# Kernel tuning notes

Hardware: AMD Instinct MI355X
Metric: run time of the kernel (lower is better)

## Reference

```python
import jax, jax.numpy as jnp
import numpy as np

N_NODES = 10000
N_EDGES = 320000
D = 128  # feature dim for edges, nodes, globals


def setup_inputs() -> dict:
    key = jax.random.key(0)
    ks = jax.random.split(key, 8)
    edges = jax.random.normal(ks[0], (N_EDGES, D), dtype=jnp.float32)
    nodes = jax.random.normal(ks[1], (N_NODES, D), dtype=jnp.float32)
    globals_ = jax.random.normal(ks[2], (D,), dtype=jnp.float32)
    receivers = jax.random.randint(ks[3], (N_EDGES,), 0, N_NODES, dtype=jnp.int32).astype(jnp.int64)
    senders = jax.random.randint(ks[4], (N_EDGES,), 0, N_NODES, dtype=jnp.int32).astype(jnp.int64)
    W1 = jax.random.normal(ks[5], (4 * D, 256), dtype=jnp.float32) * (1.0 / np.sqrt(4 * D))
    b1 = jnp.zeros((256,), dtype=jnp.float32)
    W2 = jax.random.normal(ks[6], (256, D), dtype=jnp.float32) * (1.0 / np.sqrt(256))
    b2 = jnp.zeros((D,), dtype=jnp.float32)
    return {"edges": edges, "nodes": nodes, "globals_": globals_,
            "receivers": receivers, "senders": senders,
            "W1": W1, "b1": b1, "W2": W2, "b2": b2}


def reference(edges, nodes, globals_, receivers, senders, W1, b1, W2, b2):
    # Gather adjacent node features to edges, broadcast globals, concat.
    recv_feats = nodes[receivers]                 # [E, D]
    send_feats = nodes[senders]                   # [E, D]
    glob_feats = jnp.broadcast_to(globals_, (edges.shape[0], globals_.shape[0]))  # [E, D]
    x = jnp.concatenate([edges, recv_feats, send_feats, glob_feats], axis=-1)     # [E, 4D]
    # Edge-update MLP: 4D -> 256 -> D with relu.
    h = jax.nn.relu(x @ W1 + b1)
    new_edges = h @ W2 + b2                       # [E, D]
    return new_edges
```

## Files before the change

### kernel.cpp

```cpp
#include <hip/hip_runtime.h>
#include <hip/hip_bf16.h>

#define D 128
#define NH 256
#define BM 64
#define E_TOTAL 320000
#define NNODES 10000

typedef __attribute__((ext_vector_type(8))) short bf16x8;
typedef __attribute__((ext_vector_type(4))) float f32x4;

__device__ __forceinline__ unsigned short f2b(float f) {
  unsigned int u = __builtin_bit_cast(unsigned int, f);
  u += 0x7fffu + ((u >> 16) & 1u);
  return (unsigned short)(u >> 16);
}
__device__ __forceinline__ unsigned pk2(float a, float b) {
  return (unsigned)f2b(a) | ((unsigned)f2b(b) << 16);
}
__device__ __forceinline__ uint4 pack8(float4 a, float4 b) {
  uint4 r;
  r.x = pk2(a.x, a.y); r.y = pk2(a.z, a.w);
  r.z = pk2(b.x, b.y); r.w = pk2(b.z, b.w);
  return r;
}
__device__ __forceinline__ float lo2f(unsigned u) {
  return __builtin_bit_cast(float, u << 16);
}
__device__ __forceinline__ float hi2f(unsigned u) {
  return __builtin_bit_cast(float, u & 0xffff0000u);
}
__device__ __forceinline__ void gload16(const void* g, void* l) {
  __builtin_amdgcn_global_load_lds(
      (const __attribute__((address_space(1))) void*)g,
      (__attribute__((address_space(3))) void*)l, 16, 0, 0);
}

__global__ void prep_kernel(const float* __restrict__ W1,
                            const float* __restrict__ W2,
                            const float* __restrict__ b1,
                            const float* __restrict__ g,
                            ushort* __restrict__ W1pk,
                            ushort* __restrict__ W2p,
                            float* __restrict__ cvec) {
  const int b = blockIdx.x;
  const int tid = threadIdx.x;
  if (b < 48) {
    int c = b * 256 + tid;
    int s = c >> 12;
    int rem = c & 4095;
    int nt = rem >> 8;
    int rem2 = rem & 255;
    int ks = rem2 >> 6;
    int l = rem2 & 63;
    int col = nt * 16 + (l & 15);
    int k0 = s * 128 + ks * 32 + (l >> 4) * 8;
    ushort* dst = W1pk + (size_t)c * 8;
    #pragma unroll
    for (int j = 0; j < 8; ++j)
      dst[j] = f2b(W1[(size_t)(k0 + j) * NH + col]);
  } else if (b < 64) {
    int c = (b - 48) * 256 + tid;
    int nt2 = c / (8 * 64);
    int rem = c % (8 * 64);
    int ks = rem >> 6;
    int l = rem & 63;
    int col = nt2 * 16 + (l & 15);
    int k0 = ks * 32 + (l >> 4) * 8;
    ushort* dst = W2p + (size_t)c * 8;
    #pragma unroll
    for (int j = 0; j < 8; ++j)
      dst[j] = f2b(W2[(size_t)(k0 + j) * D + col]);
  } else {
    int n = tid;
    float acc = b1[n];
    for (int k = 0; k < D; ++k)
      acc += g[k] * W1[(size_t)(384 + k) * NH + n];
    cvec[n] = acc;
  }
}

__global__ __launch_bounds__(512, 4) void nodeh_kernel(
    const float* __restrict__ nodes,
    const ushort* __restrict__ W1pk,
    const float* __restrict__ cvec,
    ushort* __restrict__ tblR,
    ushort* __restrict__ tblS) {
  __shared__ char Xn[BM * 256];
  const int role = blockIdx.y;
  ushort* __restrict__ tbl = role ? tblS : tblR;
  const int nb = blockIdx.x * BM;
  const int tid = threadIdx.x;

  {
    int row = tid >> 4;
    int cc = (tid & 15) * 16;
    #pragma unroll
    for (int q = 0; q < 2; ++q) {
      int r = row + q * 32;
      int rg = nb + r; if (rg >= NNODES) rg = NNODES - 1;
      const float* np = nodes + (size_t)rg * D + (tid & 15) * 8;
      float4 u0 = *(const float4*)np;
      float4 u1 = *(const float4*)(np + 4);
      *(uint4*)(Xn + r * 256 + (cc ^ ((r & 7) << 4))) = pack8(u0, u1);
    }
  }
  __syncthreads();

  const int lane = tid & 63;
  const int wave = tid >> 6;
  const int lr = lane & 15;
  const int kg = lane >> 4;

  const ushort* wb = W1pk + (size_t)(1 + role) * 32768
                   + (size_t)(wave * 2) * 2048 + lane * 8;
  f32x4 acc[2][4] = {};
  bf16x8 aw[2][2];
  #pragma unroll
  for (int ht = 0; ht < 2; ++ht)
    aw[0][ht] = *(const bf16x8*)(wb + ht * 2048);

  #pragma unroll
  for (int ks = 0; ks < 4; ++ks) {
    const int cur = ks & 1, nxt = cur ^ 1;
    if (ks < 3) {
      #pragma unroll
      for (int ht = 0; ht < 2; ++ht)
        aw[nxt][ht] = *(const bf16x8*)(wb + ht * 2048 + (ks + 1) * 512);
    }
    const int k0 = ks * 32 + kg * 8;
    bf16x8 xb[4];
    #pragma unroll
    for (int et = 0; et < 4; ++et) {
      int row = et * 16 + lr;
      xb[et] = *(const bf16x8*)(Xn + row * 256 + ((k0 * 2) ^ ((row & 7) << 4)));
    }
    #pragma unroll
    for (int ht = 0; ht < 2; ++ht)
      #pragma unroll
      for (int et = 0; et < 4; ++et)
        acc[ht][et] = __builtin_amdgcn_mfma_f32_16x16x32_bf16(aw[cur][ht], xb[et], acc[ht][et], 0, 0, 0);
  }

  #pragma unroll
  for (int ht = 0; ht < 2; ++ht) {
    int h0 = wave * 32 + ht * 16 + kg * 4;
    float4 cvq = {0.f, 0.f, 0.f, 0.f};
    if (role == 0) cvq = *(const float4*)(cvec + h0);
    #pragma unroll
    for (int et = 0; et < 4; ++et) {
      int n = nb + et * 16 + lr;
      if (n < NNODES) {
        uint2 pk;
        pk.x = pk2(acc[ht][et][0] + cvq.x, acc[ht][et][1] + cvq.y);
        pk.y = pk2(acc[ht][et][2] + cvq.z, acc[ht][et][3] + cvq.w);
        *(uint2*)(tbl + (size_t)n * NH + h0) = pk;
      }
    }
  }
}

__global__ __launch_bounds__(512, 4) void fused_kernel(
    const float* __restrict__ edges,
    const int* __restrict__ receivers,
    const int* __restrict__ senders,
    const ushort* __restrict__ W1pk,
    const ushort* __restrict__ tblR,
    const ushort* __restrict__ tblS,
    const ushort* __restrict__ W2p,
    const float* __restrict__ b2,
    float* __restrict__ out) {
  __shared__ char Xs[BM * 256];
  __shared__ char Hr[BM * 512];
  __shared__ char Hsb[BM * 512];

  const int ebase = blockIdx.x * BM;
  const int tid = threadIdx.x;
  const int lane = tid & 63;
  const int wave = tid >> 6;

  {
    const int wslice = wave & 3;
    const int isS = wave >> 2;
    const int* __restrict__ myarr = isS ? senders : receivers;
    const char* mytbl = (const char*)(isS ? tblS : tblR);
    char* myLds = isS ? Hsb : Hr;
    const int half = lane >> 5;
    const int ch16 = (lane & 31) * 16;
    #pragma unroll
    for (int j = 0; j < 8; ++j) {
      int r = wslice * 16 + 2 * j + half;
      int idx = myarr[ebase + r];
      gload16(mytbl + (size_t)idx * 512 + (ch16 ^ ((r & 7) << 4)),
              myLds + (wslice * 16 + 2 * j) * 512);
    }
  }

  const int erow = tid >> 4;
  const int ecc = (tid & 15) * 16;
  {
    const float* ep0 = edges + (size_t)(ebase + erow) * D + (tid & 15) * 8;
    float4 e0 = *(const float4*)ep0;
    float4 e1 = *(const float4*)(ep0 + 4);
    const float* ep1 = edges + (size_t)(ebase + erow + 32) * D + (tid & 15) * 8;
    float4 e2 = *(const float4*)ep1;
    float4 e3 = *(const float4*)(ep1 + 4);
    *(uint4*)(Xs + erow * 256 + (ecc ^ ((erow & 7) << 4))) = pack8(e0, e1);
    int r2 = erow + 32;
    *(uint4*)(Xs + r2 * 256 + (ecc ^ ((r2 & 7) << 4))) = pack8(e2, e3);
  }
  __syncthreads();

  const int lr = lane & 15;
  const int kg = lane >> 4;

  const ushort* w1base = W1pk + (size_t)(wave * 2) * 2048 + lane * 8;
  f32x4 acc[2][4] = {};
  bf16x8 aw[2][2];
  #pragma unroll
  for (int ht = 0; ht < 2; ++ht)
    aw[0][ht] = *(const bf16x8*)(w1base + ht * 2048);

  #pragma unroll
  for (int ks = 0; ks < 4; ++ks) {
    const int cur = ks & 1, nxt = cur ^ 1;
    if (ks < 3) {
      #pragma unroll
      for (int ht = 0; ht < 2; ++ht)
        aw[nxt][ht] = *(const bf16x8*)(w1base + ht * 2048 + (ks + 1) * 512);
    }
    const int k0 = ks * 32 + kg * 8;
    bf16x8 xb[4];
    #pragma unroll
    for (int et = 0; et < 4; ++et) {
      int row = et * 16 + lr;
      xb[et] = *(const bf16x8*)(Xs + row * 256 + ((k0 * 2) ^ ((row & 7) << 4)));
    }
    #pragma unroll
    for (int ht = 0; ht < 2; ++ht)
      #pragma unroll
      for (int et = 0; et < 4; ++et)
        acc[ht][et] = __builtin_amdgcn_mfma_f32_16x16x32_bf16(aw[ks & 1][ht], xb[et], acc[ht][et], 0, 0, 0);
  }

  const int wm3 = wave >> 1;
  const int wn3 = wave & 1;
  const ushort* w2base = W2p + (size_t)(wm3 * 2) * 8 * 512 + lane * 8;
  bf16x8 aw2[2][2];
  #pragma unroll
  for (int mt = 0; mt < 2; ++mt)
    aw2[0][mt] = *(const bf16x8*)(w2base + (size_t)mt * 8 * 512);

  const int h0 = wave * 32 + kg * 4;
  #pragma unroll
  for (int ht = 0; ht < 2; ++ht) {
    const int h0b = (h0 + ht * 16) * 2;
    #pragma unroll
    for (int et = 0; et < 4; ++et) {
      int e = et * 16 + lr;
      int ad = e * 512 + (h0b ^ ((e & 7) << 4));
      uint2 gr = *(uint2*)(Hr + ad);
      uint2 gs = *(uint2*)(Hsb + ad);
      float v0 = acc[ht][et][0] + lo2f(gr.x) + lo2f(gs.x);
      float v1 = acc[ht][et][1] + hi2f(gr.x) + hi2f(gs.x);
      float v2 = acc[ht][et][2] + lo2f(gr.y) + lo2f(gs.y);
      float v3 = acc[ht][et][3] + hi2f(gr.y) + hi2f(gs.y);
      v0 = v0 > 0.f ? v0 : 0.f;
      v1 = v1 > 0.f ? v1 : 0.f;
      v2 = v2 > 0.f ? v2 : 0.f;
      v3 = v3 > 0.f ? v3 : 0.f;
      uint2 pk;
      pk.x = pk2(v0, v1);
      pk.y = pk2(v2, v3);
      *(uint2*)(Hr + ad) = pk;
    }
  }
  __syncthreads();

  float4 ba = *(const float4*)(b2 + wm3 * 32 + kg * 4);
  float4 bb2 = *(const float4*)(b2 + wm3 * 32 + 16 + kg * 4);
  f32x4 acc2[2][2] = {};
  #pragma unroll
  for (int ks = 0; ks < 8; ++ks) {
    const int cur = ks & 1, nxt = cur ^ 1;
    if (ks < 7) {
      #pragma unroll
      for (int mt = 0; mt < 2; ++mt)
        aw2[nxt][mt] = *(const bf16x8*)(w2base + (size_t)mt * 8 * 512 + (ks + 1) * 512);
    }
    const int k0 = ks * 32 + kg * 8;
    bf16x8 hb[2];
    #pragma unroll
    for (int et2 = 0; et2 < 2; ++et2) {
      int e = wn3 * 32 + et2 * 16 + lr;
      hb[et2] = *(const bf16x8*)(Hr + e * 512 + ((k0 * 2) ^ ((e & 7) << 4)));
    }
    #pragma unroll
    for (int mt = 0; mt < 2; ++mt)
      #pragma unroll
      for (int et2 = 0; et2 < 2; ++et2)
        acc2[mt][et2] = __builtin_amdgcn_mfma_f32_16x16x32_bf16(aw2[cur][mt], hb[et2], acc2[mt][et2], 0, 0, 0);
  }

  #pragma unroll
  for (int mt = 0; mt < 2; ++mt) {
    const float4 bq = mt ? bb2 : ba;
    const int c0 = wm3 * 32 + mt * 16 + kg * 4;
    #pragma unroll
    for (int et2 = 0; et2 < 2; ++et2) {
      int e = wn3 * 32 + et2 * 16 + lr;
      float4 o;
      o.x = acc2[mt][et2][0] + bq.x;
      o.y = acc2[mt][et2][1] + bq.y;
      o.z = acc2[mt][et2][2] + bq.z;
      o.w = acc2[mt][et2][3] + bq.w;
      *(float4*)(out + (size_t)(ebase + e) * D + c0) = o;
    }
  }
}

extern "C" void kernel_launch(void* const* d_in, const int* in_sizes, int n_in,
                              void* d_out, int out_size, void* d_ws, size_t ws_size,
                              hipStream_t stream) {
  const float* edges     = (const float*)d_in[0];
  const float* nodes     = (const float*)d_in[1];
  const float* globals_  = (const float*)d_in[2];
  const int*   receivers = (const int*)d_in[3];
  const int*   senders   = (const int*)d_in[4];
  const float* W1        = (const float*)d_in[5];
  const float* b1        = (const float*)d_in[6];
  const float* W2        = (const float*)d_in[7];
  const float* b2        = (const float*)d_in[8];
  float* out = (float*)d_out;

  char* ws = (char*)d_ws;
  ushort* W1pk = (ushort*)ws;
  ushort* W2p  = (ushort*)(ws + 196608);
  float*  cvec = (float*)(ws + 262144);
  ushort* tblR = (ushort*)(ws + 263168);
  ushort* tblS = (ushort*)(ws + 5383168);

  hipLaunchKernelGGL(prep_kernel, dim3(65), dim3(256), 0, stream,
                     W1, W2, b1, globals_, W1pk, W2p, cvec);
  hipLaunchKernelGGL(nodeh_kernel, dim3((NNODES + BM - 1) / BM, 2), dim3(512), 0, stream,
                     nodes, W1pk, cvec, tblR, tblS);
  hipLaunchKernelGGL(fused_kernel, dim3(E_TOTAL / BM), dim3(512), 0, stream,
                     edges, receivers, senders, W1pk, tblR, tblS, W2p, b2, out);
}
```

Before: 148.6 us.

## Merge prep and node-table kernels; overlap gathers with first GEMM in fused kernel

Merges the weight-packing prep kernel and the node-table kernel into one launch. The node-table blocks now convert W1 from fp32 to bf16 themselves, which removes the dependency on the packed weights. The global-bias vector is no longer folded into the receiver table and is added inside the fused edge kernel instead. In the fused kernel, all W1 fragments are loaded up front and the edge-feature stage only waits on LDS counters before the first GEMM, so the async node-table gathers overlap with it; vmcnt is waited only before the gathered rows are consumed. This saves one launch and hides gather latency, at the cost of more registers and redundant weight conversion per node block.

```diff
diff --git a/kernel.cpp b/kernel.cpp
--- a/kernel.cpp
+++ b/kernel.cpp
@@ -35,18 +35,36 @@
       (const __attribute__((address_space(1))) void*)g,
       (__attribute__((address_space(3))) void*)l, 16, 0, 0);
 }
-
-__global__ void prep_kernel(const float* __restrict__ W1,
-                            const float* __restrict__ W2,
-                            const float* __restrict__ b1,
-                            const float* __restrict__ g,
-                            ushort* __restrict__ W1pk,
-                            ushort* __restrict__ W2p,
-                            float* __restrict__ cvec) {
+__device__ __forceinline__ void barrier_lgkm() {
+  asm volatile("s_waitcnt lgkmcnt(0)" ::: "memory");
+  __builtin_amdgcn_sched_barrier(0);
+  __builtin_amdgcn_s_barrier();
+  __builtin_amdgcn_sched_barrier(0);
+}
+__device__ __forceinline__ void barrier_vm0() {
+  asm volatile("s_waitcnt vmcnt(0) lgkmcnt(0)" ::: "memory");
+  __builtin_amdgcn_sched_barrier(0);
+  __builtin_amdgcn_s_barrier();
+  __builtin_amdgcn_sched_barrier(0);
+}
+
+__global__ __launch_bounds__(512, 4) void prep_nodeh_kernel(
+    const float* __restrict__ nodes,
+    const float* __restrict__ W1,
+    const float* __restrict__ W2,
+    const float* __restrict__ b1,
+    const float* __restrict__ g,
+    ushort* __restrict__ W1pk,
+    ushort* __restrict__ W2p,
+    float* __restrict__ cvec,
+    ushort* __restrict__ tblR,
+    ushort* __restrict__ tblS) {
+  __shared__ char Xn[BM * 256];
   const int b = blockIdx.x;
   const int tid = threadIdx.x;
-  if (b < 48) {
-    int c = b * 256 + tid;
+
+  if (b < 24) {
+    int c = b * 512 + tid;
     int s = c >> 12;
     int rem = c & 4095;
     int nt = rem >> 8;
@@ -59,8 +77,10 @@
     #pragma unroll
     for (int j = 0; j < 8; ++j)
       dst[j] = f2b(W1[(size_t)(k0 + j) * NH + col]);
-  } else if (b < 64) {
-    int c = (b - 48) * 256 + tid;
+    return;
+  }
+  if (b < 32) {
+    int c = (b - 24) * 512 + tid;
     int nt2 = c / (8 * 64);
     int rem = c % (8 * 64);
     int ks = rem >> 6;
@@ -71,26 +91,23 @@
     #pragma unroll
     for (int j = 0; j < 8; ++j)
       dst[j] = f2b(W2[(size_t)(k0 + j) * D + col]);
-  } else {
-    int n = tid;
-    float acc = b1[n];
-    for (int k = 0; k < D; ++k)
-      acc += g[k] * W1[(size_t)(384 + k) * NH + n];
-    cvec[n] = acc;
-  }
-}
-
-__global__ __launch_bounds__(512, 4) void nodeh_kernel(
-    const float* __restrict__ nodes,
-    const ushort* __restrict__ W1pk,
-    const float* __restrict__ cvec,
-    ushort* __restrict__ tblR,
-    ushort* __restrict__ tblS) {
-  __shared__ char Xn[BM * 256];
-  const int role = blockIdx.y;
+    return;
+  }
+  if (b == 32) {
+    if (tid < 256) {
+      int n = tid;
+      float acc = b1[n];
+      for (int k = 0; k < D; ++k)
+        acc += g[k] * W1[(size_t)(384 + k) * NH + n];
+      cvec[n] = acc;
+    }
+    return;
+  }
+
+  const int bi = b - 33;
+  const int role = bi >= 157;
   ushort* __restrict__ tbl = role ? tblS : tblR;
-  const int nb = blockIdx.x * BM;
-  const int tid = threadIdx.x;
+  const int nb = (bi - role * 157) * BM;
 
   {
     int row = tid >> 4;
@@ -111,23 +128,24 @@
   const int wave = tid >> 6;
   const int lr = lane & 15;
   const int kg = lane >> 4;
-
-  const ushort* wb = W1pk + (size_t)(1 + role) * 32768
-                   + (size_t)(wave * 2) * 2048 + lane * 8;
+  const int col = wave * 32 + lr;
+
+  bf16x8 aw[4][2];
+  #pragma unroll
+  for (int ks = 0; ks < 4; ++ks)
+    #pragma unroll
+    for (int ht = 0; ht < 2; ++ht) {
+      int k0 = (1 + role) * 128 + ks * 32 + kg * 8;
+      bf16x8 fr;
+      #pragma unroll
+      for (int j = 0; j < 8; ++j)
+        fr[j] = (short)f2b(W1[(size_t)(k0 + j) * NH + col + ht * 16]);
+      aw[ks][ht] = fr;
+    }
+
   f32x4 acc[2][4] = {};
-  bf16x8 aw[2][2];
-  #pragma unroll
-  for (int ht = 0; ht < 2; ++ht)
-    aw[0][ht] = *(const bf16x8*)(wb + ht * 2048);
-
   #pragma unroll
   for (int ks = 0; ks < 4; ++ks) {
-    const int cur = ks & 1, nxt = cur ^ 1;
-    if (ks < 3) {
-      #pragma unroll
-      for (int ht = 0; ht < 2; ++ht)
-        aw[nxt][ht] = *(const bf16x8*)(wb + ht * 2048 + (ks + 1) * 512);
-    }
     const int k0 = ks * 32 + kg * 8;
     bf16x8 xb[4];
     #pragma unroll
@@ -139,21 +157,19 @@
     for (int ht = 0; ht < 2; ++ht)
       #pragma unroll
       for (int et = 0; et < 4; ++et)
-        acc[ht][et] = __builtin_amdgcn_mfma_f32_16x16x32_bf16(aw[cur][ht], xb[et], acc[ht][et], 0, 0, 0);
+        acc[ht][et] = __builtin_amdgcn_mfma_f32_16x16x32_bf16(aw[ks][ht], xb[et], acc[ht][et], 0, 0, 0);
   }
 
   #pragma unroll
   for (int ht = 0; ht < 2; ++ht) {
     int h0 = wave * 32 + ht * 16 + kg * 4;
-    float4 cvq = {0.f, 0.f, 0.f, 0.f};
-    if (role == 0) cvq = *(const float4*)(cvec + h0);
     #pragma unroll
     for (int et = 0; et < 4; ++et) {
       int n = nb + et * 16 + lr;
       if (n < NNODES) {
         uint2 pk;
-        pk.x = pk2(acc[ht][et][0] + cvq.x, acc[ht][et][1] + cvq.y);
-        pk.y = pk2(acc[ht][et][2] + cvq.z, acc[ht][et][3] + cvq.w);
+        pk.x = pk2(acc[ht][et][0], acc[ht][et][1]);
+        pk.y = pk2(acc[ht][et][2], acc[ht][et][3]);
         *(uint2*)(tbl + (size_t)n * NH + h0) = pk;
       }
     }
@@ -167,6 +183,7 @@
     const ushort* __restrict__ W1pk,
     const ushort* __restrict__ tblR,
     const ushort* __restrict__ tblS,
+    const float* __restrict__ cvec,
     const ushort* __restrict__ W2p,
     const float* __restrict__ b2,
     float* __restrict__ out) {
@@ -178,57 +195,59 @@
   const int tid = threadIdx.x;
   const int lane = tid & 63;
   const int wave = tid >> 6;
-
-  {
-    const int wslice = wave & 3;
-    const int isS = wave >> 2;
-    const int* __restrict__ myarr = isS ? senders : receivers;
-    const char* mytbl = (const char*)(isS ? tblS : tblR);
-    char* myLds = isS ? Hsb : Hr;
-    const int half = lane >> 5;
-    const int ch16 = (lane & 31) * 16;
-    #pragma unroll
-    for (int j = 0; j < 8; ++j) {
-      int r = wslice * 16 + 2 * j + half;
-      int idx = myarr[ebase + r];
-      gload16(mytbl + (size_t)idx * 512 + (ch16 ^ ((r & 7) << 4)),
-              myLds + (wslice * 16 + 2 * j) * 512);
-    }
-  }
+  const int lr = lane & 15;
+  const int kg = lane >> 4;
+
+  const int wslice = wave & 3;
+  const int isS = wave >> 2;
+  const int* __restrict__ myarr = isS ? senders : receivers;
+  const char* mytbl = (const char*)(isS ? tblS : tblR);
+  char* myLds = isS ? Hsb : Hr;
+  const int half = lane >> 5;
+  const int ch16 = (lane & 31) * 16;
+  int idx[8];
+  #pragma unroll
+  for (int j = 0; j < 8; ++j)
+    idx[j] = myarr[ebase + wslice * 16 + 2 * j + half];
+
+  const ushort* w1base = W1pk + (size_t)(wave * 2) * 2048 + lane * 8;
+  bf16x8 aw[4][2];
+  #pragma unroll
+  for (int ks = 0; ks < 4; ++ks)
+    #pragma unroll
+    for (int ht = 0; ht < 2; ++ht)
+      aw[ks][ht] = *(const bf16x8*)(w1base + ht * 2048 + ks * 512);
+
+  float4 cva = *(const float4*)(cvec + wave * 32 + kg * 4);
+  float4 cvb = *(const float4*)(cvec + wave * 32 + 16 + kg * 4);
 
   const int erow = tid >> 4;
   const int ecc = (tid & 15) * 16;
+  const float* ep0 = edges + (size_t)(ebase + erow) * D + (tid & 15) * 8;
+  float4 e0 = *(const float4*)ep0;
+  float4 e1 = *(const float4*)(ep0 + 4);
+  const float* ep1 = edges + (size_t)(ebase + erow + 32) * D + (tid & 15) * 8;
+  float4 e2 = *(const float4*)ep1;
+  float4 e3 = *(const float4*)(ep1 + 4);
+
+  #pragma unroll
+  for (int j = 0; j < 8; ++j) {
+    int r = wslice * 16 + 2 * j + half;
+    gload16(mytbl + (size_t)idx[j] * 512 + (ch16 ^ ((r & 7) << 4)),
+            myLds + (wslice * 16 + 2 * j) * 512);
+  }
+
+  *(uint4*)(Xs + erow * 256 + (ecc ^ ((erow & 7) << 4))) = pack8(e0, e1);
   {
-    const float* ep0 = edges + (size_t)(ebase + erow) * D + (tid & 15) * 8;
-    float4 e0 = *(const float4*)ep0;
-    float4 e1 = *(const float4*)(ep0 + 4);
-    const float* ep1 = edges + (size_t)(ebase + erow + 32) * D + (tid & 15) * 8;
-    float4 e2 = *(const float4*)ep1;
-    float4 e3 = *(const float4*)(ep1 + 4);
-    *(uint4*)(Xs + erow * 256 + (ecc ^ ((erow & 7) << 4))) = pack8(e0, e1);
     int r2 = erow + 32;
     *(uint4*)(Xs + r2 * 256 + (ecc ^ ((r2 & 7) << 4))) = pack8(e2, e3);
   }
-  __syncthreads();
-
-  const int lr = lane & 15;
-  const int kg = lane >> 4;
-
-  const ushort* w1base = W1pk + (size_t)(wave * 2) * 2048 + lane * 8;
+
+  barrier_lgkm();
+
   f32x4 acc[2][4] = {};
-  bf16x8 aw[2][2];
-  #pragma unroll
-  for (int ht = 0; ht < 2; ++ht)
-    aw[0][ht] = *(const bf16x8*)(w1base + ht * 2048);
-
   #pragma unroll
   for (int ks = 0; ks < 4; ++ks) {
-    const int cur = ks & 1, nxt = cur ^ 1;
-    if (ks < 3) {
-      #pragma unroll
-      for (int ht = 0; ht < 2; ++ht)
-        aw[nxt][ht] = *(const bf16x8*)(w1base + ht * 2048 + (ks + 1) * 512);
-    }
     const int k0 = ks * 32 + kg * 8;
     bf16x8 xb[4];
     #pragma unroll
@@ -240,8 +259,10 @@
     for (int ht = 0; ht < 2; ++ht)
       #pragma unroll
       for (int et = 0; et < 4; ++et)
-        acc[ht][et] = __builtin_amdgcn_mfma_f32_16x16x32_bf16(aw[ks & 1][ht], xb[et], acc[ht][et], 0, 0, 0);
-  }
+        acc[ht][et] = __builtin_amdgcn_mfma_f32_16x16x32_bf16(aw[ks][ht], xb[et], acc[ht][et], 0, 0, 0);
+  }
+
+  barrier_vm0();
 
   const int wm3 = wave >> 1;
   const int wn3 = wave & 1;
@@ -254,6 +275,7 @@
   const int h0 = wave * 32 + kg * 4;
   #pragma unroll
   for (int ht = 0; ht < 2; ++ht) {
+    const float4 cvq = ht ? cvb : cva;
     const int h0b = (h0 + ht * 16) * 2;
     #pragma unroll
     for (int et = 0; et < 4; ++et) {
@@ -261,10 +283,10 @@
       int ad = e * 512 + (h0b ^ ((e & 7) << 4));
       uint2 gr = *(uint2*)(Hr + ad);
       uint2 gs = *(uint2*)(Hsb + ad);
-      float v0 = acc[ht][et][0] + lo2f(gr.x) + lo2f(gs.x);
-      float v1 = acc[ht][et][1] + hi2f(gr.x) + hi2f(gs.x);
-      float v2 = acc[ht][et][2] + lo2f(gr.y) + lo2f(gs.y);
-      float v3 = acc[ht][et][3] + hi2f(gr.y) + hi2f(gs.y);
+      float v0 = acc[ht][et][0] + cvq.x + lo2f(gr.x) + lo2f(gs.x);
+      float v1 = acc[ht][et][1] + cvq.y + hi2f(gr.x) + hi2f(gs.x);
+      float v2 = acc[ht][et][2] + cvq.z + lo2f(gr.y) + lo2f(gs.y);
+      float v3 = acc[ht][et][3] + cvq.w + hi2f(gr.y) + hi2f(gs.y);
       v0 = v0 > 0.f ? v0 : 0.f;
       v1 = v1 > 0.f ? v1 : 0.f;
       v2 = v2 > 0.f ? v2 : 0.f;
@@ -275,7 +297,8 @@
       *(uint2*)(Hr + ad) = pk;
     }
   }
-  __syncthreads();
+
+  barrier_lgkm();
 
   float4 ba = *(const float4*)(b2 + wm3 * 32 + kg * 4);
   float4 bb2 = *(const float4*)(b2 + wm3 * 32 + 16 + kg * 4);
@@ -340,10 +363,8 @@
   ushort* tblR = (ushort*)(ws + 263168);
   ushort* tblS = (ushort*)(ws + 5383168);
 
-  hipLaunchKernelGGL(prep_kernel, dim3(65), dim3(256), 0, stream,
-                     W1, W2, b1, globals_, W1pk, W2p, cvec);
-  hipLaunchKernelGGL(nodeh_kernel, dim3((NNODES + BM - 1) / BM, 2), dim3(512), 0, stream,
-                     nodes, W1pk, cvec, tblR, tblS);
+  hipLaunchKernelGGL(prep_nodeh_kernel, dim3(33 + 314), dim3(512), 0, stream,
+                     nodes, W1, W2, b1, globals_, W1pk, W2p, cvec, tblR, tblS);
   hipLaunchKernelGGL(fused_kernel, dim3(E_TOTAL / BM), dim3(512), 0, stream,
-                     edges, receivers, senders, W1pk, tblR, tblS, W2p, b2, out);
-}
+                     edges, receivers, senders, W1pk, tblR, tblS, cvec, W2p, b2, out);
+}
```

Measured after the change: 145.3 us. -2.2%, faster.
